# Optimization experiments

Hardware: AMD Instinct MI355X
Metric: run time of the kernel (lower is better)

## Reference

```python
import jax, jax.numpy as jnp
import numpy as np

B, T, D = 2, 4096, 768
H = 12
HD = D // H  # 64
SCALE = 1.0 / np.sqrt(HD)


def setup_inputs() -> dict:
    key = jax.random.key(0)
    k1, k2, k3 = jax.random.split(key, 3)
    x = jax.random.normal(k1, (B, T, D), dtype=jnp.float32)
    W_qkv = jax.random.normal(k2, (D, 3 * D), dtype=jnp.float32) * (1.0 / np.sqrt(D))
    b_qkv = jnp.zeros((3 * D,), dtype=jnp.float32)
    W_out = jax.random.normal(k3, (D, D), dtype=jnp.float32) * (1.0 / np.sqrt(D))
    b_out = jnp.zeros((D,), dtype=jnp.float32)
    return {"x": x, "W_qkv": W_qkv, "b_qkv": b_qkv, "W_out": W_out, "b_out": b_out}


def reference(x, W_qkv, b_qkv, W_out, b_out):
    Bx, Tx, C = x.shape
    qkv = x @ W_qkv + b_qkv                                  # [B,T,3D]
    qkv = qkv.reshape(Bx, Tx, 3, H, HD).transpose(2, 0, 3, 1, 4)  # [3,B,H,T,hd]
    q, k, v = qkv[0], qkv[1], qkv[2]
    scores = jnp.einsum('bhqd,bhkd->bhqk', q, k) * SCALE      # [B,H,T,T]
    causal = jnp.tril(jnp.ones((Tx, Tx), dtype=bool))
    scores = jnp.where(causal[None, None], scores, -jnp.inf)
    attn = jax.nn.softmax(scores, axis=-1)
    out = jnp.einsum('bhqk,bhkd->bhqd', attn, v)              # [B,H,T,hd]
    out = out.transpose(0, 2, 1, 3).reshape(Bx, Tx, C)        # [B,T,D]
    return out @ W_out + b_out
```

## Files before the change

kernel.cpp:

```cpp
#include <hip/hip_runtime.h>
#include <cstdint>
#include <cstddef>

typedef _Float16 f16x8 __attribute__((ext_vector_type(8)));
typedef _Float16 f16x4 __attribute__((ext_vector_type(4)));
typedef float    f32x4 __attribute__((ext_vector_type(4)));

#define AS_GLOBAL __attribute__((address_space(1)))
#define AS_LDS    __attribute__((address_space(3)))

__device__ __forceinline__ void load16_to_lds(const _Float16* g, _Float16* l) {
    __builtin_amdgcn_global_load_lds((const AS_GLOBAL void*)g, (AS_LDS void*)l, 16, 0, 0);
}

#define BB   2
#define TT   4096
#define DD   768
#define NH   12
#define HDIM 64
#define D3   2304
#define SC2  (0.125f * 1.44269504088896f)

__global__ __launch_bounds__(256) void prep(const float* __restrict__ x,
                                            _Float16* __restrict__ Xh,
                                            const float* __restrict__ Wqkv,
                                            _Float16* __restrict__ Wqkvt,
                                            const float* __restrict__ Wout,
                                            _Float16* __restrict__ Wot) {
    const int bid = blockIdx.x, tid = threadIdx.x;
    if (bid < 6144) {
        const int i = bid * 1024 + tid * 4;
        float4 v = *(const float4*)(x + i);
        f16x4 h;
        h[0] = (_Float16)v.x; h[1] = (_Float16)v.y;
        h[2] = (_Float16)v.z; h[3] = (_Float16)v.w;
        *(f16x4*)(Xh + i) = h;
        return;
    }
    __shared__ float tile[32][33];
    const float* in; _Float16* out; int C, bx, by;
    if (bid < 7872) {
        const int t = bid - 6144;
        in = Wqkv; out = Wqkvt; C = 2304;
        bx = (t % 72) * 32; by = (t / 72) * 32;
    } else {
        const int t = bid - 7872;
        in = Wout; out = Wot; C = 768;
        bx = (t % 24) * 32; by = (t / 24) * 32;
    }
    const int R = 768;
    const int tx = tid & 31, ty = tid >> 5;
#pragma unroll
    for (int j = 0; j < 32; j += 8)
        tile[ty + j][tx] = in[(size_t)(by + ty + j) * C + bx + tx];
    __syncthreads();
#pragma unroll
    for (int j = 0; j < 32; j += 8)
        out[(size_t)(bx + ty + j) * R + by + tx] = (_Float16)tile[tx][ty + j];
}

template <typename OutT>
__device__ __forceinline__ void gemm_body(const _Float16* __restrict__ A,
                                          const _Float16* __restrict__ Bt,
                                          const float* __restrict__ bias, bool bias_row,
                                          OutT* __restrict__ C, int N, int K,
                                          int m0, int n0,
                                          _Float16* As, _Float16* Bs) {
    const int tid  = threadIdx.x;
    const int wave = tid >> 6, lane = tid & 63, quad = lane >> 4, l16 = lane & 15;
    const int wm = (wave & 1) * 64, wn = (wave >> 1) * 64;
    const int rowc = lane >> 3, part = lane & 7;

    f32x4 acc[4][4];
#pragma unroll
    for (int i = 0; i < 4; ++i)
#pragma unroll
        for (int n = 0; n < 4; ++n) acc[i][n] = f32x4{0.f, 0.f, 0.f, 0.f};

    for (int k0 = 0; k0 < K; k0 += 64) {
        __syncthreads();
#pragma unroll
        for (int cc = 0; cc < 4; ++cc) {
            const int ch = wave * 4 + cc;
            load16_to_lds(A  + (size_t)(m0 + ch * 8 + rowc) * K + k0 + part * 8,
                          As + ch * 512);
            load16_to_lds(Bt + (size_t)(n0 + ch * 8 + rowc) * K + k0 + part * 8,
                          Bs + ch * 512);
        }
        __syncthreads();
#pragma unroll
        for (int i = 0; i < 4; ++i) {
            f16x8 a0 = *(const f16x8*)(As + (wm + i * 16 + l16) * 64 + quad * 8);
            f16x8 a1 = *(const f16x8*)(As + (wm + i * 16 + l16) * 64 + 32 + quad * 8);
#pragma unroll
            for (int n = 0; n < 4; ++n) {
                f16x8 b0 = *(const f16x8*)(Bs + (wn + n * 16 + l16) * 64 + quad * 8);
                f16x8 b1 = *(const f16x8*)(Bs + (wn + n * 16 + l16) * 64 + 32 + quad * 8);
                acc[i][n] = __builtin_amdgcn_mfma_f32_16x16x32_f16(a0, b0, acc[i][n], 0, 0, 0);
                acc[i][n] = __builtin_amdgcn_mfma_f32_16x16x32_f16(a1, b1, acc[i][n], 0, 0, 0);
            }
        }
    }
#pragma unroll
    for (int i = 0; i < 4; ++i)
#pragma unroll
        for (int n = 0; n < 4; ++n)
#pragma unroll
            for (int r = 0; r < 4; ++r) {
                const int row = m0 + wm + i * 16 + quad * 4 + r;
                const int col = n0 + wn + n * 16 + l16;
                const float bv = bias_row ? bias[row] : bias[col];
                C[(size_t)row * N + col] = (OutT)(acc[i][n][r] + bv);
            }
}

__global__ __launch_bounds__(256) void gemm_qkv(const _Float16* __restrict__ Xh,
                                                const _Float16* __restrict__ Wqkvt,
                                                const float* __restrict__ bqkv,
                                                _Float16* __restrict__ QKh,
                                                _Float16* __restrict__ VtG) {
    __shared__ __align__(16) _Float16 As[128 * 64];
    __shared__ __align__(16) _Float16 Bs[128 * 64];
    const int bid = blockIdx.x;
    if (bid < 768) {
        const int bx = bid % 12, by = bid / 12;
        gemm_body<_Float16>(Xh, Wqkvt, bqkv, false, QKh, 1536, DD,
                            by * 128, bx * 128, As, Bs);
    } else {
        const int t = bid - 768;
        const int bx = t % 64, by = t / 64;
        gemm_body<_Float16>(Wqkvt + (size_t)1536 * DD, Xh, bqkv + 1536, true, VtG,
                            8192, DD, by * 128, bx * 128, As, Bs);
    }
}

__global__ __launch_bounds__(256) void gemm_out(const _Float16* __restrict__ A,
                                                const _Float16* __restrict__ Bt,
                                                const float* __restrict__ bias,
                                                float* __restrict__ C) {
    __shared__ __align__(16) _Float16 As[128 * 64];
    __shared__ __align__(16) _Float16 Bs[128 * 64];
    gemm_body<float>(A, Bt, bias, false, C, DD, DD,
                     (int)blockIdx.y * 128, (int)blockIdx.x * 128, As, Bs);
}

__global__ __launch_bounds__(256, 5) void attn_kernel(const _Float16* __restrict__ qk,
                                                      const _Float16* __restrict__ vt,
                                                      _Float16* __restrict__ ao) {
    __shared__ __align__(16) _Float16 Ks[2][64 * 64];
    __shared__ __align__(16) _Float16 Vs[2][64 * 64];

    const int L    = blockIdx.x;
    const int xcd  = L & 7;
    const int r_   = L >> 3;
    const int gIdx = r_ % 3;
    const int qt   = 63 - r_ / 3;
    const int g    = gIdx * 8 + xcd;
    const int b = g / NH, h = g % NH;

    const int tid = threadIdx.x;
    const int wave = tid >> 6, lane = tid & 63, quad = lane >> 4, l16 = lane & 15;
    const int wq = wave >> 1, wk = wave & 1;

    f16x4 ones4;
#pragma unroll
    for (int j = 0; j < 4; ++j) ones4[j] = (_Float16)1.0f;

    int vK[2], vV[2];
#pragma unroll
    for (int p = 0; p < 2; ++p) {
        const int j   = wave * 16 + p * 8 + (lane >> 3);
        const int cdk = (lane & 7) ^ (j & 7);
        vK[p] = (b * TT + j) * 1536 + DD + h * HDIM + cdk * 8;
        vV[p] = (h * HDIM + j) * 8192 + b * TT + cdk * 8;
    }
    auto stage = [&](int buf, int k0) {
        const int kK = k0 * 1536;
#pragma unroll
        for (int p = 0; p < 2; ++p) {
            load16_to_lds(qk + (vK[p] + kK), Ks[buf] + (wave * 16 + p * 8) * 64);
            load16_to_lds(vt + (vV[p] + k0), Vs[buf] + (wave * 16 + p * 8) * 64);
        }
    };

    const int q0 = qt * 64;
    const int nkt = qt + 1;
    const int qrow0 = q0 + wq * 32;
    const int qr_lane = qrow0 + l16;
    f16x8 aq[2][2];
#pragma unroll
    for (int mq = 0; mq < 2; ++mq) {
        const int qoff = (b * TT + qrow0 + mq * 16 + l16) * 1536 + h * HDIM + quad * 8;
        const _Float16 sc = (_Float16)SC2;
        aq[mq][0] = *(const f16x8*)(qk + qoff) * sc;
        aq[mq][1] = *(const f16x8*)(qk + qoff + 32) * sc;
    }
    f32x4 o[2][4], lac[2];
#pragma unroll
    for (int mq = 0; mq < 2; ++mq) {
#pragma unroll
        for (int n = 0; n < 4; ++n) o[mq][n] = f32x4{0.f, 0.f, 0.f, 0.f};
        lac[mq] = f32x4{0.f, 0.f, 0.f, 0.f};
    }

    stage(0, 0);
    int cur = 0;
    for (int kt = 0; kt < nkt; ++kt) {
        __syncthreads();
        if (kt + 1 < nkt) stage(cur ^ 1, (kt + 1) * 64);

        __builtin_amdgcn_s_setprio(1);
        f32x4 s[2][2];
#pragma unroll
        for (int mq = 0; mq < 2; ++mq)
#pragma unroll
            for (int n1 = 0; n1 < 2; ++n1) s[mq][n1] = f32x4{0.f, 0.f, 0.f, 0.f};
#pragma unroll
        for (int kh = 0; kh < 2; ++kh)
#pragma unroll
            for (int n1 = 0; n1 < 2; ++n1) {
                const int rowK = (wk * 2 + n1) * 16 + l16;
                const int pos = (kh * 4 + quad) ^ (l16 & 7);
                f16x8 bk = *(const f16x8*)(Ks[cur] + rowK * 64 + pos * 8);
                s[0][n1] = __builtin_amdgcn_mfma_f32_16x16x32_f16(bk, aq[0][kh], s[0][n1], 0, 0, 0);
                s[1][n1] = __builtin_amdgcn_mfma_f32_16x16x32_f16(bk, aq[1][kh], s[1][n1], 0, 0, 0);
            }
        __builtin_amdgcn_s_setprio(0);

        if (kt == nkt - 1) {
#pragma unroll
            for (int mq = 0; mq < 2; ++mq) {
                const int qr = qr_lane + mq * 16;
#pragma unroll
                for (int n1 = 0; n1 < 2; ++n1) {
                    const int kg0 = kt * 64 + wk * 32 + n1 * 16 + quad * 4;
#pragma unroll
                    for (int r = 0; r < 4; ++r)
                        if (kg0 + r > qr) s[mq][n1][r] = -1e30f;
                }
            }
        }

        f16x4 pa[2][2];
#pragma unroll
        for (int mq = 0; mq < 2; ++mq)
#pragma unroll
            for (int n1 = 0; n1 < 2; ++n1)
#pragma unroll
                for (int r = 0; r < 4; ++r)
                    pa[mq][n1][r] = (_Float16)__builtin_amdgcn_exp2f(s[mq][n1][r]);

        __builtin_amdgcn_s_setprio(1);
#pragma unroll
        for (int mq = 0; mq < 2; ++mq) {
            lac[mq] = __builtin_amdgcn_mfma_f32_16x16x16f16(pa[mq][0], ones4, lac[mq], 0, 0, 0);
            lac[mq] = __builtin_amdgcn_mfma_f32_16x16x16f16(pa[mq][1], ones4, lac[mq], 0, 0, 0);
        }
#pragma unroll
        for (int n1 = 0; n1 < 2; ++n1)
#pragma unroll
            for (int n = 0; n < 4; ++n) {
                const int rowV = n * 16 + l16;
                const int lc  = wk * 4 + n1 * 2 + (quad >> 1);
                const int pc  = lc ^ (l16 & 7);
                f16x4 bv = *(const f16x4*)(Vs[cur] + rowV * 64 + pc * 8 + (quad & 1) * 4);
                o[0][n] = __builtin_amdgcn_mfma_f32_16x16x16f16(pa[0][n1], bv, o[0][n], 0, 0, 0);
                o[1][n] = __builtin_amdgcn_mfma_f32_16x16x16f16(pa[1][n1], bv, o[1][n], 0, 0, 0);
            }
        __builtin_amdgcn_s_setprio(0);
        cur ^= 1;
    }

    __syncthreads();
    float* const Ksf = (float*)&Ks[0][0];
    float* const Vsf = (float*)&Vs[0][0];
    if (wk) {
#pragma unroll
        for (int mq = 0; mq < 2; ++mq) {
            if (l16 == 0)
                *(f32x4*)(Vsf + wq * 32 + mq * 16 + quad * 4) = lac[mq];
#pragma unroll
            for (int n = 0; n < 4; ++n)
                *(f32x4*)(Ksf + wq * 2048 + (mq * 4 + n) * 256 + lane * 4) = o[mq][n];
        }
    }
    __syncthreads();
    if (!wk) {
#pragma unroll
        for (int mq = 0; mq < 2; ++mq) {
            f32x4 lp = *(const f32x4*)(Vsf + wq * 32 + mq * 16 + quad * 4);
            f32x4 inv;
#pragma unroll
            for (int r = 0; r < 4; ++r) inv[r] = 1.0f / (lac[mq][r] + lp[r]);
#pragma unroll
            for (int n = 0; n < 4; ++n) {
                f32x4 op = *(const f32x4*)(Ksf + wq * 2048 + (mq * 4 + n) * 256 + lane * 4);
#pragma unroll
                for (int r = 0; r < 4; ++r) {
                    const int ooff = (b * TT + qrow0 + mq * 16 + quad * 4 + r) * DD + h * HDIM + l16;
                    ao[ooff + n * 16] = (_Float16)((o[mq][n][r] + op[r]) * inv[r]);
                }
            }
        }
    }
}

extern "C" void kernel_launch(void* const* d_in, const int* in_sizes, int n_in,
                              void* d_out, int out_size, void* d_ws, size_t ws_size,
                              hipStream_t stream) {
    const float* x     = (const float*)d_in[0];
    const float* Wqkv  = (const float*)d_in[1];
    const float* bqkv  = (const float*)d_in[2];
    const float* Wout  = (const float*)d_in[3];
    const float* bout  = (const float*)d_in[4];
    float* out = (float*)d_out;

    char* ws = (char*)d_ws;
    _Float16* Xh    = (_Float16*)ws;  ws += (size_t)BB * TT * DD * 2;
    _Float16* Wqkvt = (_Float16*)ws;  ws += (size_t)D3 * DD * 2;
    _Float16* Wot   = (_Float16*)ws;  ws += (size_t)DD * DD * 2;
    _Float16* QKh   = (_Float16*)ws;  ws += (size_t)BB * TT * 1536 * 2;
    _Float16* VtG   = (_Float16*)ws;  ws += (size_t)DD * BB * TT * 2;
    _Float16* AOh   = (_Float16*)ws;  ws += (size_t)BB * TT * DD * 2;

    prep<<<8448, 256, 0, stream>>>(x, Xh, Wqkv, Wqkvt, Wout, Wot);

    gemm_qkv<<<1152, 256, 0, stream>>>(Xh, Wqkvt, bqkv, QKh, VtG);

    attn_kernel<<<1536, 256, 0, stream>>>(QKh, VtG, AOh);

    gemm_out<<<dim3(DD / 128, (BB * TT) / 128), 256, 0, stream>>>(AOh, Wot, bout, out);
}
```

Before: 241.2 us.

## Fuse fp32-to-fp16 conversion of x into QKV GEMM and shrink output GEMM tile

Removes the separate conversion pass that wrote an fp16 copy of x. The QKV GEMM now loads fp32 x directly and converts it to fp16 on the way into LDS, replacing the async global-to-LDS path for that operand. The output projection GEMM gets its own kernel with 64-row M tiles, doubling the block count to 768 for better CU occupancy. The trade-off is that x is read at twice the byte width, and more than once across tiles, through registers instead of direct LDS loads.

After: 244.7 us. No clear change (+1.4%).

```diff
diff --git a/kernel.cpp b/kernel.cpp
--- a/kernel.cpp
+++ b/kernel.cpp
@@ -21,30 +21,19 @@
 #define D3   2304
 #define SC2  (0.125f * 1.44269504088896f)
 
-__global__ __launch_bounds__(256) void prep(const float* __restrict__ x,
-                                            _Float16* __restrict__ Xh,
-                                            const float* __restrict__ Wqkv,
+__global__ __launch_bounds__(256) void prep(const float* __restrict__ Wqkv,
                                             _Float16* __restrict__ Wqkvt,
                                             const float* __restrict__ Wout,
                                             _Float16* __restrict__ Wot) {
     const int bid = blockIdx.x, tid = threadIdx.x;
-    if (bid < 6144) {
-        const int i = bid * 1024 + tid * 4;
-        float4 v = *(const float4*)(x + i);
-        f16x4 h;
-        h[0] = (_Float16)v.x; h[1] = (_Float16)v.y;
-        h[2] = (_Float16)v.z; h[3] = (_Float16)v.w;
-        *(f16x4*)(Xh + i) = h;
-        return;
-    }
     __shared__ float tile[32][33];
     const float* in; _Float16* out; int C, bx, by;
-    if (bid < 7872) {
-        const int t = bid - 6144;
+    if (bid < 1728) {
+        const int t = bid;
         in = Wqkv; out = Wqkvt; C = 2304;
         bx = (t % 72) * 32; by = (t / 72) * 32;
     } else {
-        const int t = bid - 7872;
+        const int t = bid - 1728;
         in = Wout; out = Wot; C = 768;
         bx = (t % 24) * 32; by = (t / 24) * 32;
     }
@@ -59,9 +48,11 @@
         out[(size_t)(bx + ty + j) * R + by + tx] = (_Float16)tile[tx][ty + j];
 }
 
-template <typename OutT>
+template <typename OutT, bool CA, bool CB>
 __device__ __forceinline__ void gemm_body(const _Float16* __restrict__ A,
+                                          const float* __restrict__ A32,
                                           const _Float16* __restrict__ Bt,
+                                          const float* __restrict__ B32,
                                           const float* __restrict__ bias, bool bias_row,
                                           OutT* __restrict__ C, int N, int K,
                                           int m0, int n0,
@@ -82,10 +73,34 @@
 #pragma unroll
         for (int cc = 0; cc < 4; ++cc) {
             const int ch = wave * 4 + cc;
-            load16_to_lds(A  + (size_t)(m0 + ch * 8 + rowc) * K + k0 + part * 8,
-                          As + ch * 512);
-            load16_to_lds(Bt + (size_t)(n0 + ch * 8 + rowc) * K + k0 + part * 8,
-                          Bs + ch * 512);
+            if constexpr (CA) {
+                const float* src = A32 + (size_t)(m0 + ch * 8 + rowc) * K + k0 + part * 8;
+                float4 v0 = *(const float4*)src;
+                float4 v1 = *(const float4*)(src + 4);
+                f16x8 hv;
+                hv[0] = (_Float16)v0.x; hv[1] = (_Float16)v0.y;
+                hv[2] = (_Float16)v0.z; hv[3] = (_Float16)v0.w;
+                hv[4] = (_Float16)v1.x; hv[5] = (_Float16)v1.y;
+                hv[6] = (_Float16)v1.z; hv[7] = (_Float16)v1.w;
+                *(f16x8*)(As + ch * 512 + rowc * 64 + part * 8) = hv;
+            } else {
+                load16_to_lds(A + (size_t)(m0 + ch * 8 + rowc) * K + k0 + part * 8,
+                              As + ch * 512);
+            }
+            if constexpr (CB) {
+                const float* src = B32 + (size_t)(n0 + ch * 8 + rowc) * K + k0 + part * 8;
+                float4 v0 = *(const float4*)src;
+                float4 v1 = *(const float4*)(src + 4);
+                f16x8 hv;
+                hv[0] = (_Float16)v0.x; hv[1] = (_Float16)v0.y;
+                hv[2] = (_Float16)v0.z; hv[3] = (_Float16)v0.w;
+                hv[4] = (_Float16)v1.x; hv[5] = (_Float16)v1.y;
+                hv[6] = (_Float16)v1.z; hv[7] = (_Float16)v1.w;
+                *(f16x8*)(Bs + ch * 512 + rowc * 64 + part * 8) = hv;
+            } else {
+                load16_to_lds(Bt + (size_t)(n0 + ch * 8 + rowc) * K + k0 + part * 8,
+                              Bs + ch * 512);
+            }
         }
         __syncthreads();
 #pragma unroll
@@ -114,7 +129,7 @@
             }
 }
 
-__global__ __launch_bounds__(256) void gemm_qkv(const _Float16* __restrict__ Xh,
+__global__ __launch_bounds__(256) void gemm_qkv(const float* __restrict__ x,
                                                 const _Float16* __restrict__ Wqkvt,
                                                 const float* __restrict__ bqkv,
                                                 _Float16* __restrict__ QKh,
@@ -124,13 +139,14 @@
     const int bid = blockIdx.x;
     if (bid < 768) {
         const int bx = bid % 12, by = bid / 12;
-        gemm_body<_Float16>(Xh, Wqkvt, bqkv, false, QKh, 1536, DD,
-                            by * 128, bx * 128, As, Bs);
+        gemm_body<_Float16, true, false>(nullptr, x, Wqkvt, nullptr, bqkv, false,
+                                         QKh, 1536, DD, by * 128, bx * 128, As, Bs);
     } else {
         const int t = bid - 768;
         const int bx = t % 64, by = t / 64;
-        gemm_body<_Float16>(Wqkvt + (size_t)1536 * DD, Xh, bqkv + 1536, true, VtG,
-                            8192, DD, by * 128, bx * 128, As, Bs);
+        gemm_body<_Float16, false, true>(Wqkvt + (size_t)1536 * DD, nullptr, nullptr, x,
+                                         bqkv + 1536, true, VtG,
+                                         8192, DD, by * 128, bx * 128, As, Bs);
     }
 }
 
@@ -138,10 +154,59 @@
                                                 const _Float16* __restrict__ Bt,
                                                 const float* __restrict__ bias,
                                                 float* __restrict__ C) {
-    __shared__ __align__(16) _Float16 As[128 * 64];
+    __shared__ __align__(16) _Float16 As[64 * 64];
     __shared__ __align__(16) _Float16 Bs[128 * 64];
-    gemm_body<float>(A, Bt, bias, false, C, DD, DD,
-                     (int)blockIdx.y * 128, (int)blockIdx.x * 128, As, Bs);
+    const int m0 = (int)blockIdx.y * 64, n0 = (int)blockIdx.x * 128;
+    const int N = DD, K = DD;
+    const int tid  = threadIdx.x;
+    const int wave = tid >> 6, lane = tid & 63, quad = lane >> 4, l16 = lane & 15;
+    const int wm = (wave & 1) * 32, wn = (wave >> 1) * 64;
+    const int rowc = lane >> 3, part = lane & 7;
+
+    f32x4 acc[2][4];
+#pragma unroll
+    for (int i = 0; i < 2; ++i)
+#pragma unroll
+        for (int n = 0; n < 4; ++n) acc[i][n] = f32x4{0.f, 0.f, 0.f, 0.f};
+
+    for (int k0 = 0; k0 < K; k0 += 64) {
+        __syncthreads();
+#pragma unroll
+        for (int cc = 0; cc < 2; ++cc) {
+            const int ch = wave * 2 + cc;
+            load16_to_lds(A + (size_t)(m0 + ch * 8 + rowc) * K + k0 + part * 8,
+                          As + ch * 512);
+        }
+#pragma unroll
+        for (int cc = 0; cc < 4; ++cc) {
+            const int ch = wave * 4 + cc;
+            load16_to_lds(Bt + (size_t)(n0 + ch * 8 + rowc) * K + k0 + part * 8,
+                          Bs + ch * 512);
+        }
+        __syncthreads();
+#pragma unroll
+        for (int i = 0; i < 2; ++i) {
+            f16x8 a0 = *(const f16x8*)(As + (wm + i * 16 + l16) * 64 + quad * 8);
+            f16x8 a1 = *(const f16x8*)(As + (wm + i * 16 + l16) * 64 + 32 + quad * 8);
+#pragma unroll
+            for (int n = 0; n < 4; ++n) {
+                f16x8 b0 = *(const f16x8*)(Bs + (wn + n * 16 + l16) * 64 + quad * 8);
+                f16x8 b1 = *(const f16x8*)(Bs + (wn + n * 16 + l16) * 64 + 32 + quad * 8);
+                acc[i][n] = __builtin_amdgcn_mfma_f32_16x16x32_f16(a0, b0, acc[i][n], 0, 0, 0);
+                acc[i][n] = __builtin_amdgcn_mfma_f32_16x16x32_f16(a1, b1, acc[i][n], 0, 0, 0);
+            }
+        }
+    }
+#pragma unroll
+    for (int i = 0; i < 2; ++i)
+#pragma unroll
+        for (int n = 0; n < 4; ++n)
+#pragma unroll
+            for (int r = 0; r < 4; ++r) {
+                const int row = m0 + wm + i * 16 + quad * 4 + r;
+                const int col = n0 + wn + n * 16 + l16;
+                C[(size_t)row * N + col] = acc[i][n][r] + bias[col];
+            }
 }
 
 __global__ __launch_bounds__(256, 5) void attn_kernel(const _Float16* __restrict__ qk,
@@ -316,18 +381,17 @@
     float* out = (float*)d_out;
 
     char* ws = (char*)d_ws;
-    _Float16* Xh    = (_Float16*)ws;  ws += (size_t)BB * TT * DD * 2;
     _Float16* Wqkvt = (_Float16*)ws;  ws += (size_t)D3 * DD * 2;
     _Float16* Wot   = (_Float16*)ws;  ws += (size_t)DD * DD * 2;
     _Float16* QKh   = (_Float16*)ws;  ws += (size_t)BB * TT * 1536 * 2;
     _Float16* VtG   = (_Float16*)ws;  ws += (size_t)DD * BB * TT * 2;
     _Float16* AOh   = (_Float16*)ws;  ws += (size_t)BB * TT * DD * 2;
 
-    prep<<<8448, 256, 0, stream>>>(x, Xh, Wqkv, Wqkvt, Wout, Wot);
-
-    gemm_qkv<<<1152, 256, 0, stream>>>(Xh, Wqkvt, bqkv, QKh, VtG);
+    prep<<<2304, 256, 0, stream>>>(Wqkv, Wqkvt, Wout, Wot);
+
+    gemm_qkv<<<1152, 256, 0, stream>>>(x, Wqkvt, bqkv, QKh, VtG);
 
     attn_kernel<<<1536, 256, 0, stream>>>(QKh, VtG, AOh);
 
-    gemm_out<<<dim3(DD / 128, (BB * TT) / 128), 256, 0, stream>>>(AOh, Wot, bout, out);
-}
+    gemm_out<<<dim3(DD / 128, (BB * TT) / 64), 256, 0, stream>>>(AOh, Wot, bout, out);
+}
```
